# Optimization experiments

Hardware: AMD Instinct MI355X
Metric: run time of the kernel (lower is better)

Reference implementation:

```python
import jax, jax.numpy as jnp
import numpy as np

B, S, D, H, DC, HC = 2, 2048, 1024, 16, 64, 16  # batch, seq, hidden, heads, coord_dim, head_coord_dim
HD = D // H  # head_dim


def setup_inputs() -> dict:
    key = jax.random.key(0)
    ks = jax.random.split(key, 12)
    s = lambda fan_in: 1.0 / np.sqrt(fan_in)
    return {
        "hidden_states": jax.random.normal(ks[0], (B, S, D), jnp.float32),
        "coordinates": jax.random.normal(ks[1], (B, S, DC), jnp.float32),
        # weights stored [in, out] (used as x @ W + b, equivalent to torch Linear)
        "Wv": jax.random.uniform(ks[2], (D, D), jnp.float32, -s(D), s(D)),
        "bv": jax.random.uniform(ks[3], (D,), jnp.float32, -s(D), s(D)),
        "Wc": jax.random.uniform(ks[4], (DC, H * HC), jnp.float32, -s(DC), s(DC)),
        "bc": jax.random.uniform(ks[5], (H * HC,), jnp.float32, -s(DC), s(DC)),
        "Wn": jax.random.uniform(ks[6], (DC, DC), jnp.float32, -s(DC), s(DC)),
        "bn": jax.random.uniform(ks[7], (DC,), jnp.float32, -s(DC), s(DC)),
        "Wo": jax.random.uniform(ks[8], (D, D), jnp.float32, -s(D), s(D)),
        "bo": jax.random.uniform(ks[9], (D,), jnp.float32, -s(D), s(D)),
        "gamma": jax.random.normal(ks[10], (1, H, 1, 1), jnp.float32),
    }


def reference(hidden_states, coordinates, Wv, bv, Wc, bc, Wn, bn, Wo, bo, gamma):
    b, s, _ = hidden_states.shape
    # value: [B,H,S,HD]
    value = (hidden_states @ Wv + bv).reshape(b, s, H, HD).transpose(0, 2, 1, 3)
    # coord heads: [B,H,S,HC]
    z = (coordinates @ Wc + bc).reshape(b, s, H, HC).transpose(0, 2, 1, 3)
    z_sq = jnp.sum(z * z, axis=-1, keepdims=True)  # [B,H,S,1]
    sq_dist = z_sq + jnp.swapaxes(z_sq, -1, -2) - 2.0 * jnp.einsum("bhsc,bhtc->bhst", z, z)
    sq_dist = jnp.maximum(sq_dist, 0.0)
    g = jax.nn.softplus(gamma)  # [1,H,1,1]
    attn = jax.nn.softmax(-g * sq_dist, axis=-1)  # [B,H,S,S]
    out = jnp.einsum("bhst,bhtd->bhsd", attn, value)
    out = out.transpose(0, 2, 1, 3).reshape(b, s, D)
    updated_hidden = out @ Wo + bo
    updated_coords = coordinates @ Wn + bn
    return (updated_hidden, updated_coords)
```

## Files before the change

### kernel.cpp

```cpp
#include <hip/hip_runtime.h>
#include <hip/hip_bf16.h>

typedef short bf16x8 __attribute__((ext_vector_type(8)));
typedef float f32x4 __attribute__((ext_vector_type(4)));
typedef float f32x16 __attribute__((ext_vector_type(16)));
typedef unsigned short u16;
typedef unsigned int u32;

__device__ __forceinline__ u16 f2b(float f) {
  __hip_bfloat16 h = __float2bfloat16(f);
  return *reinterpret_cast<u16*>(&h);
}

#define MFMA16(a, b, c) __builtin_amdgcn_mfma_f32_16x16x32_bf16((a), (b), (c), 0, 0, 0)
#define MFMA32(a, b, c) __builtin_amdgcn_mfma_f32_32x32x16_bf16((a), (b), (c), 0, 0, 0)


__global__ void k_cvt(const float* __restrict__ in, u16* __restrict__ out, int n) {
  int i = (blockIdx.x * 256 + threadIdx.x) * 4;
  if (i >= n) return;
  float4 v = *reinterpret_cast<const float4*>(in + i);
  ushort4 o;
  o.x = f2b(v.x); o.y = f2b(v.y); o.z = f2b(v.z); o.w = f2b(v.w);
  *reinterpret_cast<ushort4*>(out + i) = o;
}

__global__ void k_wT(const float* __restrict__ W, u16* __restrict__ WT) {
  __shared__ float t[64][65];
  int tid = threadIdx.x;
  int r0 = (blockIdx.x & 15) << 6;
  int c0 = (blockIdx.x >> 4) << 6;
#pragma unroll
  for (int rep = 0; rep < 4; ++rep) {
    int e = tid + rep * 256;
    int r = e >> 4, c4 = (e & 15) << 2;
    float4 v = *reinterpret_cast<const float4*>(W + (size_t)(r0 + r) * 1024 + c0 + c4);
    t[r][c4] = v.x; t[r][c4 + 1] = v.y; t[r][c4 + 2] = v.z; t[r][c4 + 3] = v.w;
  }
  __syncthreads();
#pragma unroll
  for (int rep = 0; rep < 4; ++rep) {
    int e = tid + rep * 256;
    int c = e >> 4, r4 = (e & 15) << 2;
    ushort4 o;
    o.x = f2b(t[r4][c]); o.y = f2b(t[r4 + 1][c]);
    o.z = f2b(t[r4 + 2][c]); o.w = f2b(t[r4 + 3][c]);
    *reinterpret_cast<ushort4*>(WT + (size_t)(c0 + c) * 1024 + r0 + r4) = o;
  }
}

__global__ void k_z(const float* __restrict__ C, const float* __restrict__ Wc,
                    const float* __restrict__ bc, u16* __restrict__ Z,
                    float* __restrict__ zsq) {
  int gid = blockIdx.x * 256 + threadIdx.x;
  int bs = gid >> 4, h = gid & 15;
  const float* crow = C + (size_t)bs * 64;
  float acc[16];
#pragma unroll
  for (int c = 0; c < 16; ++c) acc[c] = bc[h * 16 + c];
  for (int k = 0; k < 64; ++k) {
    float cv = crow[k];
    const float* wr = Wc + (size_t)k * 256 + h * 16;
#pragma unroll
    for (int c = 0; c < 16; ++c) acc[c] = fmaf(cv, wr[c], acc[c]);
  }
  float sq = 0.f;
  u16 tmp[16];
#pragma unroll
  for (int c = 0; c < 16; ++c) { sq += acc[c] * acc[c]; tmp[c] = f2b(acc[c]); }
  int b = bs >> 11, s = bs & 2047;
  int bh = (b << 4) + h;
  u16* zr = Z + (((size_t)bh << 11) + s) * 16;
  *reinterpret_cast<uint4*>(zr) = *reinterpret_cast<uint4*>(tmp);
  *reinterpret_cast<uint4*>(zr + 8) = *reinterpret_cast<uint4*>(tmp + 8);
  zsq[((size_t)bh << 11) + s] = sq;
}

template <int OUTM>
__global__ __launch_bounds__(256) void k_gemm(const u16* __restrict__ A,
                                              const u16* __restrict__ BT,
                                              const float* __restrict__ bias,
                                              void* __restrict__ Cout,
                                              int M, int N, int K) {
  __shared__ u16 As[128 * 64];
  __shared__ u16 Bs[64 * 64];
  int nbn = N >> 6;
  int bm = blockIdx.x / nbn, bn = blockIdx.x % nbn;
  int tid = threadIdx.x, lane = tid & 63, w = tid >> 6;
  int wm = w >> 1, wn = w & 1;
  int l15 = lane & 15, lg = lane >> 4;
  int lr = lane >> 3;
  int swc = (lane & 7) ^ lr;

  f32x4 acc[4][2];
#pragma unroll
  for (int mi = 0; mi < 4; ++mi)
#pragma unroll
    for (int ni = 0; ni < 2; ++ni) acc[mi][ni] = (f32x4){0.f, 0.f, 0.f, 0.f};

  const u16* Abase = A + (size_t)(bm * 128) * K + (size_t)(w * 8 + lr) * K + swc * 8;
  const u16* Bbase = BT + (size_t)(bn * 64) * K + (size_t)(w * 8 + lr) * K + swc * 8;
  int rsw = l15 & 7;

  for (int kk0 = 0; kk0 < K; kk0 += 64) {
    __syncthreads();
#pragma unroll
    for (int i = 0; i < 4; ++i)
      __builtin_amdgcn_global_load_lds(
          (const __attribute__((address_space(1))) u32*)(Abase + (size_t)(i * 32) * K + kk0),
          (__attribute__((address_space(3))) u32*)&As[(i * 32 + w * 8) * 64], 16, 0, 0);
#pragma unroll
    for (int i = 0; i < 2; ++i)
      __builtin_amdgcn_global_load_lds(
          (const __attribute__((address_space(1))) u32*)(Bbase + (size_t)(i * 32) * K + kk0),
          (__attribute__((address_space(3))) u32*)&Bs[(i * 32 + w * 8) * 64], 16, 0, 0);
    __syncthreads();
#pragma unroll
    for (int kk = 0; kk < 2; ++kk) {
      bf16x8 af[4], bfr[2];
#pragma unroll
      for (int mi = 0; mi < 4; ++mi) {
        int row = wm * 64 + mi * 16 + l15;
        int ch = (kk * 4 + lg) ^ rsw;
        af[mi] = *reinterpret_cast<const bf16x8*>(&As[row * 64 + ch * 8]);
      }
#pragma unroll
      for (int ni = 0; ni < 2; ++ni) {
        int row = wn * 32 + ni * 16 + l15;
        int ch = (kk * 4 + lg) ^ rsw;
        bfr[ni] = *reinterpret_cast<const bf16x8*>(&Bs[row * 64 + ch * 8]);
      }
#pragma unroll
      for (int mi = 0; mi < 4; ++mi)
#pragma unroll
        for (int ni = 0; ni < 2; ++ni)
          acc[mi][ni] = MFMA16(af[mi], bfr[ni], acc[mi][ni]);
    }
  }
#pragma unroll
  for (int mi = 0; mi < 4; ++mi) {
#pragma unroll
    for (int ni = 0; ni < 2; ++ni) {
      int col = bn * 64 + wn * 32 + ni * 16 + l15;
      float bb = bias[col];
#pragma unroll
      for (int j = 0; j < 4; ++j) {
        int row = bm * 128 + wm * 64 + mi * 16 + lg * 4 + j;
        float v = acc[mi][ni][j] + bb;
        if (OUTM == 0) {
          reinterpret_cast<float*>(Cout)[(size_t)row * N + col] = v;
        } else {
          int b = row >> 11, s = row & 2047, h = col >> 6, hd = col & 63;
          reinterpret_cast<u16*>(Cout)[((((size_t)(b * 16 + h) << 11) | s) << 6) + hd] = f2b(v);
        }
      }
    }
  }
}

__global__ void k_vF(const u16* __restrict__ V, u16* __restrict__ VF) {
  __shared__ u16 t[64][72];
  int tid = threadIdx.x;
  int bh = blockIdx.x >> 5;
  int s0 = (blockIdx.x & 31) << 6;
#pragma unroll
  for (int rep = 0; rep < 2; ++rep) {
    int e = tid + rep * 256;
    int sl = e >> 3, seg = (e & 7) << 3;
    *reinterpret_cast<uint4*>(&t[sl][seg]) =
        *reinterpret_cast<const uint4*>(V + ((size_t)(bh * 2048 + s0 + sl) << 6) + seg);
  }
  __syncthreads();
  int tg0 = (blockIdx.x & 31) << 2;
#pragma unroll
  for (int rep = 0; rep < 2; ++rep) {
    int c = tid + rep * 256;
    int l = c & 63;
    int dh = (c >> 6) & 1;
    int tgl = c >> 7;
    int l31 = l & 31, hi = l >> 5;
    u16 tmp[8];
#pragma unroll
    for (int j = 0; j < 8; ++j) tmp[j] = t[tgl * 16 + hi * 8 + j][dh * 32 + l31];
    size_t off = ((((size_t)bh * 128 + tg0 + tgl) * 2 + dh) << 9) + (l << 3);
    *reinterpret_cast<uint4*>(VF + off) = *reinterpret_cast<uint4*>(tmp);
  }
}

__global__ __launch_bounds__(256, 4) void k_attn(const u16* __restrict__ Z,
                                                 const float* __restrict__ zsq,
                                                 const u16* __restrict__ VF,
                                                 const float* __restrict__ gamma,
                                                 u16* __restrict__ O) {
  __shared__ __align__(16) char smem[18944];
  float* psqf = reinterpret_cast<float*>(smem + 18432);

  int tid = threadIdx.x, lane = tid & 63, w = tid >> 6;
  int l31 = lane & 31, hi = lane >> 5;
  int hi4 = hi << 2, hi8 = hi << 3;
  int th = w >> 1, qh = w & 1, th32 = th << 5;
  int bh = blockIdx.x >> 5, qt = blockIdx.x & 31;
  int q0 = qt << 6;
  int h = bh & 15, bb = bh >> 4;
  float gm = gamma[h];
  float g = (gm > 15.f) ? gm : log1pf(__expf(gm));
  float g2 = g * 1.4426950408889634f;

  const u16* Zb = Z + ((size_t)bh << 11) * 16;
  const float* zsb = zsq + ((size_t)bh << 11);
  const u16* VFb = VF + ((size_t)bh << 17);

  int q = (qh << 5) + l31;
  char* Prow = smem + q * 144;
  u32 psw = ((u32)(q >> 3) & 3u) << 4;

  uint4 zqu = *reinterpret_cast<const uint4*>(Zb + (size_t)(q0 + q) * 16 + hi8);
  zqu.x += 0x00800080u; zqu.y += 0x00800080u;
  zqu.z += 0x00800080u; zqu.w += 0x00800080u;
  bf16x8 zq2 = *reinterpret_cast<bf16x8*>(&zqu);

  bf16x8 aug_b;
  {
    float xq = -zsb[q0 + q];
    u32 xqu = __float_as_uint(xq);
    float xqh = __uint_as_float(xqu & 0xFFFF0000u);
    float xql = xq - xqh;
    u32 w1q = __builtin_amdgcn_perm(__float_as_uint(xql), xqu, 0x07060302u);
    uint4 abu = {0x3F803F80u, w1q, 0u, 0u};
    if (hi) { abu.x = 0u; abu.y = 0u; }
    aug_b = *reinterpret_cast<bf16x8*>(&abu);
  }

  const u16* zap = Zb + (size_t)(th32 + l31) * 16 + hi8;
  const float* xtp = zsb + th32 + l31;
  const u16* vwp = VFb + ((size_t)(th * 2) << 10) + (lane << 3);

  f32x16 oacc0 = {}, oacc1 = {};
  f32x4 psacc = {};

  bf16x8 zA_c = *reinterpret_cast<const bf16x8*>(zap);
  float zs_c = xtp[0];
  bf16x8 vb00_c = *reinterpret_cast<const bf16x8*>(vwp);
  bf16x8 vb10_c = *reinterpret_cast<const bf16x8*>(vwp + 512);

#pragma unroll 2
  for (int tt = 0; tt < 32; ++tt) {
    const int t0 = tt << 6;
    char* Pr = Prow + ((tt & 1) ? 9216 : 0);
    const u16* vtb = vwp + (tt << 12);
    bf16x8 vb01 = *reinterpret_cast<const bf16x8*>(vtb + 1024);
    bf16x8 vb11 = *reinterpret_cast<const bf16x8*>(vtb + 1024 + 512);
    bf16x8 zA_n = zA_c, vb00_n = vb00_c, vb10_n = vb10_c;
    float zs_n = zs_c;
    if (tt < 31) {
      zA_n = *reinterpret_cast<const bf16x8*>(zap + (size_t)(t0 + 64) * 16);
      zs_n = xtp[t0 + 64];
      vb00_n = *reinterpret_cast<const bf16x8*>(vtb + 4096);
      vb10_n = *reinterpret_cast<const bf16x8*>(vtb + 4096 + 512);
    }

    float xt = -zs_c;
    u32 xtu = __float_as_uint(xt);
    float xth = __uint_as_float(xtu & 0xFFFF0000u);
    float xtl = xt - xth;
    u32 w0 = __builtin_amdgcn_perm(__float_as_uint(xtl), xtu, 0x07060302u);
    uint4 aau = {w0, 0x3F803F80u, 0u, 0u};
    if (hi) { aau.x = 0u; aau.y = 0u; }
    bf16x8 aug_a = *reinterpret_cast<bf16x8*>(&aau);

    f32x16 sc = MFMA32(aug_a, aug_b, (f32x16){});
    sc = MFMA32(zA_c, zq2, sc);

#pragma unroll
    for (int g4 = 0; g4 < 4; ++g4) {
      float e0 = fminf(g2 * sc[g4 * 4 + 0], 0.f);
      float e1 = fminf(g2 * sc[g4 * 4 + 1], 0.f);
      float e2 = fminf(g2 * sc[g4 * 4 + 2], 0.f);
      float e3 = fminf(g2 * sc[g4 * 4 + 3], 0.f);
      float p0 = __builtin_amdgcn_exp2f(e0);
      float p1 = __builtin_amdgcn_exp2f(e1);
      float p2 = __builtin_amdgcn_exp2f(e2);
      float p3 = __builtin_amdgcn_exp2f(e3);
      psacc[0] += p0; psacc[1] += p1; psacc[2] += p2; psacc[3] += p3;
      u32 pk0, pk1;
      asm("v_cvt_pk_bf16_f32 %0, %1, %2" : "=v"(pk0) : "v"(p0), "v"(p1));
      asm("v_cvt_pk_bf16_f32 %0, %1, %2" : "=v"(pk1) : "v"(p2), "v"(p3));
      uint2 pkv = {pk0, pk1};
      int tcol = th32 + (g4 << 3) + hi4;
      *reinterpret_cast<uint2*>(Pr + (((u32)(tcol << 1)) ^ psw)) = pkv;
    }

    bf16x8 pa0 = *reinterpret_cast<const bf16x8*>(Pr + (((u32)((th32 + hi8) << 1)) ^ psw));
    bf16x8 pa1 = *reinterpret_cast<const bf16x8*>(Pr + (((u32)((th32 + 16 + hi8) << 1)) ^ psw));

    oacc0 = MFMA32(pa0, vb00_c, oacc0);
    oacc1 = MFMA32(pa0, vb10_c, oacc1);
    oacc0 = MFMA32(pa1, vb01, oacc0);
    oacc1 = MFMA32(pa1, vb11, oacc1);

    zA_c = zA_n; zs_c = zs_n; vb00_c = vb00_n; vb10_c = vb10_n;
  }

  float psum = (psacc[0] + psacc[1]) + (psacc[2] + psacc[3]);

  psum += __shfl_xor(psum, 32, 64);
  __syncthreads();
  if (w >= 2) {
    char* dst = smem + (w - 2) * 8192 + lane * 16;
#pragma unroll
    for (int c = 0; c < 4; ++c) {
      f32x4 v = {oacc0[c * 4 + 0], oacc0[c * 4 + 1], oacc0[c * 4 + 2], oacc0[c * 4 + 3]};
      *reinterpret_cast<f32x4*>(dst + c * 1024) = v;
    }
#pragma unroll
    for (int c = 0; c < 4; ++c) {
      f32x4 v = {oacc1[c * 4 + 0], oacc1[c * 4 + 1], oacc1[c * 4 + 2], oacc1[c * 4 + 3]};
      *reinterpret_cast<f32x4*>(dst + (c + 4) * 1024) = v;
    }
  }
  if (lane < 32) psqf[w * 32 + l31] = psum;
  __syncthreads();
  if (w < 2) {
    const char* src = smem + w * 8192 + lane * 16;
#pragma unroll
    for (int c = 0; c < 4; ++c) {
      f32x4 v = *reinterpret_cast<const f32x4*>(src + c * 1024);
      oacc0[c * 4 + 0] += v[0]; oacc0[c * 4 + 1] += v[1];
      oacc0[c * 4 + 2] += v[2]; oacc0[c * 4 + 3] += v[3];
    }
#pragma unroll
    for (int c = 0; c < 4; ++c) {
      f32x4 v = *reinterpret_cast<const f32x4*>(src + (c + 4) * 1024);
      oacc1[c * 4 + 0] += v[0]; oacc1[c * 4 + 1] += v[1];
      oacc1[c * 4 + 2] += v[2]; oacc1[c * 4 + 3] += v[3];
    }
#pragma unroll
    for (int g4 = 0; g4 < 4; ++g4) {
      f32x4 a = *reinterpret_cast<const f32x4*>(&psqf[qh * 32 + (g4 << 3) + hi4]);
      f32x4 b2 = *reinterpret_cast<const f32x4*>(&psqf[(qh + 2) * 32 + (g4 << 3) + hi4]);
#pragma unroll
      for (int j = 0; j < 4; ++j) {
        float inv = __builtin_amdgcn_rcpf(a[j] + b2[j]);
        int qrow = (g4 << 3) + hi4 + j;
        int srow = q0 + (qh << 5) + qrow;
        u16* orow = O + ((size_t)(bb * 2048 + srow) << 10) + h * 64 + l31;
        orow[0] = f2b(oacc0[g4 * 4 + j] * inv);
        orow[32] = f2b(oacc1[g4 * 4 + j] * inv);
      }
    }
  }
}

__global__ void k_coords(const float* __restrict__ C, const float* __restrict__ Wn,
                         const float* __restrict__ bn, float* __restrict__ out) {
  int gid = blockIdx.x * 256 + threadIdx.x;
  int bs = gid >> 6, c = gid & 63;
  const float* crow = C + (size_t)bs * 64;
  float acc = bn[c];
#pragma unroll 8
  for (int k = 0; k < 64; ++k) acc = fmaf(crow[k], Wn[k * 64 + c], acc);
  out[gid] = acc;
}

extern "C" void kernel_launch(void* const* d_in, const int* in_sizes, int n_in,
                              void* d_out, int out_size, void* d_ws, size_t ws_size,
                              hipStream_t stream) {
  const float* hs     = (const float*)d_in[0];
  const float* coords = (const float*)d_in[1];
  const float* Wv     = (const float*)d_in[2];
  const float* bv     = (const float*)d_in[3];
  const float* Wc     = (const float*)d_in[4];
  const float* bc     = (const float*)d_in[5];
  const float* Wn     = (const float*)d_in[6];
  const float* bn     = (const float*)d_in[7];
  const float* Wo     = (const float*)d_in[8];
  const float* bo     = (const float*)d_in[9];
  const float* gamma  = (const float*)d_in[10];
  float* out_h = (float*)d_out;
  float* out_c = out_h + 4194304;

  char* ws = (char*)d_ws;
  u16*   HSb  = (u16*)(ws + 0);
  u16*   O    = (u16*)(ws + 0);
  u16*   WvT  = (u16*)(ws + 8388608);
  u16*   WoT  = (u16*)(ws + 10485760);
  u16*   Zw   = (u16*)(ws + 12582912);
  float* zsqw = (float*)(ws + 14680064);
  u16*   Vw   = (u16*)(ws + 14942208);
  u16*   VFw  = (u16*)(ws + 23330816);

  k_cvt<<<4096, 256, 0, stream>>>(hs, HSb, 4194304);
  k_wT<<<256, 256, 0, stream>>>(Wv, WvT);
  k_wT<<<256, 256, 0, stream>>>(Wo, WoT);
  k_z<<<256, 256, 0, stream>>>(coords, Wc, bc, Zw, zsqw);
  k_gemm<1><<<512, 256, 0, stream>>>(HSb, WvT, bv, Vw, 4096, 1024, 1024);
  k_vF<<<1024, 256, 0, stream>>>(Vw, VFw);
  k_attn<<<1024, 256, 0, stream>>>(Zw, zsqw, VFw, gamma, O);
  k_gemm<0><<<512, 256, 0, stream>>>(O, WoT, bo, out_h, 4096, 1024, 1024);
  k_coords<<<1024, 256, 0, stream>>>(coords, Wn, bn, out_c);
}
```

Baseline: 121.3 us.

## Fuse prep kernels, fold gamma into Z, and widen GEMM blocks

Merges the hidden-state conversion, both weight transposes, the coordinate-head projection and the coordinate output linear into one launch, cutting launch count from nine to five. The coordinate projection now also writes a gamma-scaled copy of Z and a packed split-bf16 of -g*|z|^2. This lets the attention loop drop its per-element gamma multiply and the per-tile norm splitting, and the query-norm term is computed once by an MFMA. Both GEMMs now run 512 threads per block so each wave holds a smaller accumulator tile. That may raise occupancy but also means fewer MFMAs per LDS load.

```diff
diff --git a/kernel.cpp b/kernel.cpp
--- a/kernel.cpp
+++ b/kernel.cpp
@@ -16,72 +16,107 @@
 #define MFMA32(a, b, c) __builtin_amdgcn_mfma_f32_32x32x16_bf16((a), (b), (c), 0, 0, 0)
 
 
-__global__ void k_cvt(const float* __restrict__ in, u16* __restrict__ out, int n) {
-  int i = (blockIdx.x * 256 + threadIdx.x) * 4;
-  if (i >= n) return;
-  float4 v = *reinterpret_cast<const float4*>(in + i);
-  ushort4 o;
-  o.x = f2b(v.x); o.y = f2b(v.y); o.z = f2b(v.z); o.w = f2b(v.w);
-  *reinterpret_cast<ushort4*>(out + i) = o;
-}
-
-__global__ void k_wT(const float* __restrict__ W, u16* __restrict__ WT) {
+__global__ __launch_bounds__(256) void k_prep(
+    const float* __restrict__ hs, u16* __restrict__ HSb,
+    const float* __restrict__ Wv, u16* __restrict__ WvT,
+    const float* __restrict__ Wo, u16* __restrict__ WoT,
+    const float* __restrict__ C, const float* __restrict__ Wc,
+    const float* __restrict__ bc, const float* __restrict__ gamma,
+    u16* __restrict__ Z, u16* __restrict__ Zg, u32* __restrict__ zghl,
+    const float* __restrict__ Wn, const float* __restrict__ bn,
+    float* __restrict__ outc) {
   __shared__ float t[64][65];
   int tid = threadIdx.x;
-  int r0 = (blockIdx.x & 15) << 6;
-  int c0 = (blockIdx.x >> 4) << 6;
-#pragma unroll
-  for (int rep = 0; rep < 4; ++rep) {
-    int e = tid + rep * 256;
-    int r = e >> 4, c4 = (e & 15) << 2;
-    float4 v = *reinterpret_cast<const float4*>(W + (size_t)(r0 + r) * 1024 + c0 + c4);
-    t[r][c4] = v.x; t[r][c4 + 1] = v.y; t[r][c4 + 2] = v.z; t[r][c4 + 3] = v.w;
-  }
-  __syncthreads();
-#pragma unroll
-  for (int rep = 0; rep < 4; ++rep) {
-    int e = tid + rep * 256;
-    int c = e >> 4, r4 = (e & 15) << 2;
+  int blk = blockIdx.x;
+
+  if (blk < 4096) {
+    int i = (blk * 256 + tid) * 4;
+    float4 v = *reinterpret_cast<const float4*>(hs + i);
     ushort4 o;
-    o.x = f2b(t[r4][c]); o.y = f2b(t[r4 + 1][c]);
-    o.z = f2b(t[r4 + 2][c]); o.w = f2b(t[r4 + 3][c]);
-    *reinterpret_cast<ushort4*>(WT + (size_t)(c0 + c) * 1024 + r0 + r4) = o;
-  }
-}
-
-__global__ void k_z(const float* __restrict__ C, const float* __restrict__ Wc,
-                    const float* __restrict__ bc, u16* __restrict__ Z,
-                    float* __restrict__ zsq) {
-  int gid = blockIdx.x * 256 + threadIdx.x;
-  int bs = gid >> 4, h = gid & 15;
-  const float* crow = C + (size_t)bs * 64;
-  float acc[16];
-#pragma unroll
-  for (int c = 0; c < 16; ++c) acc[c] = bc[h * 16 + c];
-  for (int k = 0; k < 64; ++k) {
-    float cv = crow[k];
-    const float* wr = Wc + (size_t)k * 256 + h * 16;
-#pragma unroll
-    for (int c = 0; c < 16; ++c) acc[c] = fmaf(cv, wr[c], acc[c]);
-  }
-  float sq = 0.f;
-  u16 tmp[16];
-#pragma unroll
-  for (int c = 0; c < 16; ++c) { sq += acc[c] * acc[c]; tmp[c] = f2b(acc[c]); }
-  int b = bs >> 11, s = bs & 2047;
-  int bh = (b << 4) + h;
-  u16* zr = Z + (((size_t)bh << 11) + s) * 16;
-  *reinterpret_cast<uint4*>(zr) = *reinterpret_cast<uint4*>(tmp);
-  *reinterpret_cast<uint4*>(zr + 8) = *reinterpret_cast<uint4*>(tmp + 8);
-  zsq[((size_t)bh << 11) + s] = sq;
+    o.x = f2b(v.x); o.y = f2b(v.y); o.z = f2b(v.z); o.w = f2b(v.w);
+    *reinterpret_cast<ushort4*>(HSb + i) = o;
+    return;
+  }
+  if (blk < 4608) {
+    const float* W = (blk < 4352) ? Wv : Wo;
+    u16* WT = (blk < 4352) ? WvT : WoT;
+    int bid = (blk < 4352) ? blk - 4096 : blk - 4352;
+    int r0 = (bid & 15) << 6, c0 = (bid >> 4) << 6;
+#pragma unroll
+    for (int rep = 0; rep < 4; ++rep) {
+      int e = tid + rep * 256;
+      int r = e >> 4, c4 = (e & 15) << 2;
+      float4 v = *reinterpret_cast<const float4*>(W + (size_t)(r0 + r) * 1024 + c0 + c4);
+      t[r][c4] = v.x; t[r][c4 + 1] = v.y; t[r][c4 + 2] = v.z; t[r][c4 + 3] = v.w;
+    }
+    __syncthreads();
+#pragma unroll
+    for (int rep = 0; rep < 4; ++rep) {
+      int e = tid + rep * 256;
+      int c = e >> 4, r4 = (e & 15) << 2;
+      ushort4 o;
+      o.x = f2b(t[r4][c]); o.y = f2b(t[r4 + 1][c]);
+      o.z = f2b(t[r4 + 2][c]); o.w = f2b(t[r4 + 3][c]);
+      *reinterpret_cast<ushort4*>(WT + (size_t)(c0 + c) * 1024 + r0 + r4) = o;
+    }
+    return;
+  }
+  if (blk < 4864) {
+    int gid = (blk - 4608) * 256 + tid;
+    int bs = gid >> 4, h = gid & 15;
+    float gm = gamma[h];
+    float g = (gm > 15.f) ? gm : log1pf(__expf(gm));
+    float g2 = g * 1.4426950408889634f;
+    float tg2 = 2.f * g2;
+    const float* crow = C + (size_t)bs * 64;
+    float acc[16];
+#pragma unroll
+    for (int c = 0; c < 16; ++c) acc[c] = bc[h * 16 + c];
+    for (int k = 0; k < 64; ++k) {
+      float cv = crow[k];
+      const float* wr = Wc + (size_t)k * 256 + h * 16;
+#pragma unroll
+      for (int c = 0; c < 16; ++c) acc[c] = fmaf(cv, wr[c], acc[c]);
+    }
+    float sq = 0.f;
+    u16 tz[16], tg[16];
+#pragma unroll
+    for (int c = 0; c < 16; ++c) {
+      sq += acc[c] * acc[c];
+      tz[c] = f2b(acc[c]);
+      tg[c] = f2b(tg2 * acc[c]);
+    }
+    float x = -g2 * sq;
+    u32 xu = __float_as_uint(x);
+    float xh = __uint_as_float(xu & 0xFFFF0000u);
+    u32 packed = (xu >> 16) | ((u32)f2b(x - xh) << 16);
+    int b = bs >> 11, s = bs & 2047;
+    int bh = (b << 4) + h;
+    size_t ro = (((size_t)bh << 11) + s) * 16;
+    *reinterpret_cast<uint4*>(Z + ro) = *reinterpret_cast<uint4*>(tz);
+    *reinterpret_cast<uint4*>(Z + ro + 8) = *reinterpret_cast<uint4*>(tz + 8);
+    *reinterpret_cast<uint4*>(Zg + ro) = *reinterpret_cast<uint4*>(tg);
+    *reinterpret_cast<uint4*>(Zg + ro + 8) = *reinterpret_cast<uint4*>(tg + 8);
+    zghl[((size_t)bh << 11) + s] = packed;
+    return;
+  }
+  {
+    int gid = (blk - 4864) * 256 + tid;
+    int bs = gid >> 6, c = gid & 63;
+    const float* crow = C + (size_t)bs * 64;
+    float acc = bn[c];
+#pragma unroll 8
+    for (int k = 0; k < 64; ++k) acc = fmaf(crow[k], Wn[k * 64 + c], acc);
+    outc[gid] = acc;
+  }
 }
 
 template <int OUTM>
-__global__ __launch_bounds__(256) void k_gemm(const u16* __restrict__ A,
-                                              const u16* __restrict__ BT,
-                                              const float* __restrict__ bias,
-                                              void* __restrict__ Cout,
-                                              int M, int N, int K) {
+__global__ __launch_bounds__(512, 4) void k_gemm(const u16* __restrict__ A,
+                                                 const u16* __restrict__ BT,
+                                                 const float* __restrict__ bias,
+                                                 void* __restrict__ Cout,
+                                                 int M, int N, int K) {
   __shared__ u16 As[128 * 64];
   __shared__ u16 Bs[64 * 64];
   int nbn = N >> 6;
@@ -92,60 +127,53 @@
   int lr = lane >> 3;
   int swc = (lane & 7) ^ lr;
 
-  f32x4 acc[4][2];
-#pragma unroll
-  for (int mi = 0; mi < 4; ++mi)
+  f32x4 acc[2][2];
+#pragma unroll
+  for (int mi = 0; mi < 2; ++mi)
 #pragma unroll
     for (int ni = 0; ni < 2; ++ni) acc[mi][ni] = (f32x4){0.f, 0.f, 0.f, 0.f};
 
-  const u16* Abase = A + (size_t)(bm * 128) * K + (size_t)(w * 8 + lr) * K + swc * 8;
-  const u16* Bbase = BT + (size_t)(bn * 64) * K + (size_t)(w * 8 + lr) * K + swc * 8;
+  const u16* Abase = A + (size_t)(bm * 128 + w * 8 + lr) * K + swc * 8;
+  const u16* Bbase = BT + (size_t)(bn * 64 + w * 8 + lr) * K + swc * 8;
   int rsw = l15 & 7;
 
   for (int kk0 = 0; kk0 < K; kk0 += 64) {
     __syncthreads();
 #pragma unroll
-    for (int i = 0; i < 4; ++i)
-      __builtin_amdgcn_global_load_lds(
-          (const __attribute__((address_space(1))) u32*)(Abase + (size_t)(i * 32) * K + kk0),
-          (__attribute__((address_space(3))) u32*)&As[(i * 32 + w * 8) * 64], 16, 0, 0);
-#pragma unroll
     for (int i = 0; i < 2; ++i)
       __builtin_amdgcn_global_load_lds(
-          (const __attribute__((address_space(1))) u32*)(Bbase + (size_t)(i * 32) * K + kk0),
-          (__attribute__((address_space(3))) u32*)&Bs[(i * 32 + w * 8) * 64], 16, 0, 0);
+          (const __attribute__((address_space(1))) u32*)(Abase + (size_t)(i * 64) * K + kk0),
+          (__attribute__((address_space(3))) u32*)&As[(i * 64 + w * 8) * 64], 16, 0, 0);
+    __builtin_amdgcn_global_load_lds(
+        (const __attribute__((address_space(1))) u32*)(Bbase + kk0),
+        (__attribute__((address_space(3))) u32*)&Bs[(w * 8) * 64], 16, 0, 0);
     __syncthreads();
 #pragma unroll
     for (int kk = 0; kk < 2; ++kk) {
-      bf16x8 af[4], bfr[2];
-#pragma unroll
-      for (int mi = 0; mi < 4; ++mi) {
-        int row = wm * 64 + mi * 16 + l15;
-        int ch = (kk * 4 + lg) ^ rsw;
-        af[mi] = *reinterpret_cast<const bf16x8*>(&As[row * 64 + ch * 8]);
-      }
-#pragma unroll
-      for (int ni = 0; ni < 2; ++ni) {
-        int row = wn * 32 + ni * 16 + l15;
-        int ch = (kk * 4 + lg) ^ rsw;
-        bfr[ni] = *reinterpret_cast<const bf16x8*>(&Bs[row * 64 + ch * 8]);
-      }
-#pragma unroll
-      for (int mi = 0; mi < 4; ++mi)
+      int ch = (kk * 4 + lg) ^ rsw;
+      bf16x8 af[2], bfr[2];
+#pragma unroll
+      for (int mi = 0; mi < 2; ++mi)
+        af[mi] = *reinterpret_cast<const bf16x8*>(&As[(wm * 32 + mi * 16 + l15) * 64 + ch * 8]);
+#pragma unroll
+      for (int ni = 0; ni < 2; ++ni)
+        bfr[ni] = *reinterpret_cast<const bf16x8*>(&Bs[(wn * 32 + ni * 16 + l15) * 64 + ch * 8]);
+#pragma unroll
+      for (int mi = 0; mi < 2; ++mi)
 #pragma unroll
         for (int ni = 0; ni < 2; ++ni)
           acc[mi][ni] = MFMA16(af[mi], bfr[ni], acc[mi][ni]);
     }
   }
 #pragma unroll
-  for (int mi = 0; mi < 4; ++mi) {
+  for (int mi = 0; mi < 2; ++mi) {
 #pragma unroll
     for (int ni = 0; ni < 2; ++ni) {
       int col = bn * 64 + wn * 32 + ni * 16 + l15;
       float bb = bias[col];
 #pragma unroll
       for (int j = 0; j < 4; ++j) {
-        int row = bm * 128 + wm * 64 + mi * 16 + lg * 4 + j;
+        int row = bm * 128 + wm * 32 + mi * 16 + lg * 4 + j;
         float v = acc[mi][ni][j] + bb;
         if (OUTM == 0) {
           reinterpret_cast<float*>(Cout)[(size_t)row * N + col] = v;
@@ -188,9 +216,9 @@
 }
 
 __global__ __launch_bounds__(256, 4) void k_attn(const u16* __restrict__ Z,
-                                                 const float* __restrict__ zsq,
+                                                 const u16* __restrict__ Zg,
+                                                 const u32* __restrict__ zghl,
                                                  const u16* __restrict__ VF,
-                                                 const float* __restrict__ gamma,
                                                  u16* __restrict__ O) {
   __shared__ __align__(16) char smem[18944];
   float* psqf = reinterpret_cast<float*>(smem + 18432);
@@ -202,44 +230,37 @@
   int bh = blockIdx.x >> 5, qt = blockIdx.x & 31;
   int q0 = qt << 6;
   int h = bh & 15, bb = bh >> 4;
-  float gm = gamma[h];
-  float g = (gm > 15.f) ? gm : log1pf(__expf(gm));
-  float g2 = g * 1.4426950408889634f;
 
   const u16* Zb = Z + ((size_t)bh << 11) * 16;
-  const float* zsb = zsq + ((size_t)bh << 11);
+  const u16* Zgb = Zg + ((size_t)bh << 11) * 16;
+  const u32* ghl = zghl + ((size_t)bh << 11);
   const u16* VFb = VF + ((size_t)bh << 17);
 
   int q = (qh << 5) + l31;
   char* Prow = smem + q * 144;
   u32 psw = ((u32)(q >> 3) & 3u) << 4;
 
-  uint4 zqu = *reinterpret_cast<const uint4*>(Zb + (size_t)(q0 + q) * 16 + hi8);
-  zqu.x += 0x00800080u; zqu.y += 0x00800080u;
-  zqu.z += 0x00800080u; zqu.w += 0x00800080u;
-  bf16x8 zq2 = *reinterpret_cast<bf16x8*>(&zqu);
-
-  bf16x8 aug_b;
-  {
-    float xq = -zsb[q0 + q];
-    u32 xqu = __float_as_uint(xq);
-    float xqh = __uint_as_float(xqu & 0xFFFF0000u);
-    float xql = xq - xqh;
-    u32 w1q = __builtin_amdgcn_perm(__float_as_uint(xql), xqu, 0x07060302u);
-    uint4 abu = {0x3F803F80u, w1q, 0u, 0u};
-    if (hi) { abu.x = 0u; abu.y = 0u; }
-    aug_b = *reinterpret_cast<bf16x8*>(&abu);
-  }
+  bf16x8 zq2 = *reinterpret_cast<const bf16x8*>(Zgb + (size_t)(q0 + q) * 16 + hi8);
+
+  u32 gq = ghl[q0 + q];
+  uint4 abu = {0x3F803F80u, gq, 0u, 0u};
+  if (hi) { abu.x = 0u; abu.y = 0u; }
+  bf16x8 aug_b = *reinterpret_cast<bf16x8*>(&abu);
+
+  uint4 aqu = {0u, 0x3F803F80u, 0u, 0u};
+  if (hi) aqu.y = 0u;
+  bf16x8 aug_q = *reinterpret_cast<bf16x8*>(&aqu);
+  f32x16 qpart = MFMA32(aug_q, aug_b, (f32x16){});
 
   const u16* zap = Zb + (size_t)(th32 + l31) * 16 + hi8;
-  const float* xtp = zsb + th32 + l31;
+  const u32* xtp = ghl + th32 + l31;
   const u16* vwp = VFb + ((size_t)(th * 2) << 10) + (lane << 3);
 
   f32x16 oacc0 = {}, oacc1 = {};
   f32x4 psacc = {};
 
   bf16x8 zA_c = *reinterpret_cast<const bf16x8*>(zap);
-  float zs_c = xtp[0];
+  u32 zhl_c = xtp[0];
   bf16x8 vb00_c = *reinterpret_cast<const bf16x8*>(vwp);
   bf16x8 vb10_c = *reinterpret_cast<const bf16x8*>(vwp + 512);
 
@@ -251,32 +272,26 @@
     bf16x8 vb01 = *reinterpret_cast<const bf16x8*>(vtb + 1024);
     bf16x8 vb11 = *reinterpret_cast<const bf16x8*>(vtb + 1024 + 512);
     bf16x8 zA_n = zA_c, vb00_n = vb00_c, vb10_n = vb10_c;
-    float zs_n = zs_c;
+    u32 zhl_n = zhl_c;
     if (tt < 31) {
       zA_n = *reinterpret_cast<const bf16x8*>(zap + (size_t)(t0 + 64) * 16);
-      zs_n = xtp[t0 + 64];
+      zhl_n = xtp[t0 + 64];
       vb00_n = *reinterpret_cast<const bf16x8*>(vtb + 4096);
       vb10_n = *reinterpret_cast<const bf16x8*>(vtb + 4096 + 512);
     }
 
-    float xt = -zs_c;
-    u32 xtu = __float_as_uint(xt);
-    float xth = __uint_as_float(xtu & 0xFFFF0000u);
-    float xtl = xt - xth;
-    u32 w0 = __builtin_amdgcn_perm(__float_as_uint(xtl), xtu, 0x07060302u);
-    uint4 aau = {w0, 0x3F803F80u, 0u, 0u};
-    if (hi) { aau.x = 0u; aau.y = 0u; }
+    uint4 aau = {hi ? 0u : zhl_c, 0u, 0u, 0u};
     bf16x8 aug_a = *reinterpret_cast<bf16x8*>(&aau);
 
-    f32x16 sc = MFMA32(aug_a, aug_b, (f32x16){});
+    f32x16 sc = MFMA32(aug_a, aug_b, qpart);
     sc = MFMA32(zA_c, zq2, sc);
 
 #pragma unroll
     for (int g4 = 0; g4 < 4; ++g4) {
-      float e0 = fminf(g2 * sc[g4 * 4 + 0], 0.f);
-      float e1 = fminf(g2 * sc[g4 * 4 + 1], 0.f);
-      float e2 = fminf(g2 * sc[g4 * 4 + 2], 0.f);
-      float e3 = fminf(g2 * sc[g4 * 4 + 3], 0.f);
+      float e0 = fminf(sc[g4 * 4 + 0], 0.f);
+      float e1 = fminf(sc[g4 * 4 + 1], 0.f);
+      float e2 = fminf(sc[g4 * 4 + 2], 0.f);
+      float e3 = fminf(sc[g4 * 4 + 3], 0.f);
       float p0 = __builtin_amdgcn_exp2f(e0);
       float p1 = __builtin_amdgcn_exp2f(e1);
       float p2 = __builtin_amdgcn_exp2f(e2);
@@ -298,7 +313,7 @@
     oacc0 = MFMA32(pa1, vb01, oacc0);
     oacc1 = MFMA32(pa1, vb11, oacc1);
 
-    zA_c = zA_n; zs_c = zs_n; vb00_c = vb00_n; vb10_c = vb10_n;
+    zA_c = zA_n; zhl_c = zhl_n; vb00_c = vb00_n; vb10_c = vb10_n;
   }
 
   float psum = (psacc[0] + psacc[1]) + (psacc[2] + psacc[3]);
@@ -349,17 +364,6 @@
       }
     }
   }
-}
-
-__global__ void k_coords(const float* __restrict__ C, const float* __restrict__ Wn,
-                         const float* __restrict__ bn, float* __restrict__ out) {
-  int gid = blockIdx.x * 256 + threadIdx.x;
-  int bs = gid >> 6, c = gid & 63;
-  const float* crow = C + (size_t)bs * 64;
-  float acc = bn[c];
-#pragma unroll 8
-  for (int k = 0; k < 64; ++k) acc = fmaf(crow[k], Wn[k * 64 + c], acc);
-  out[gid] = acc;
 }
 
 extern "C" void kernel_launch(void* const* d_in, const int* in_sizes, int n_in,
@@ -385,17 +389,15 @@
   u16*   WvT  = (u16*)(ws + 8388608);
   u16*   WoT  = (u16*)(ws + 10485760);
   u16*   Zw   = (u16*)(ws + 12582912);
-  float* zsqw = (float*)(ws + 14680064);
-  u16*   Vw   = (u16*)(ws + 14942208);
-  u16*   VFw  = (u16*)(ws + 23330816);
-
-  k_cvt<<<4096, 256, 0, stream>>>(hs, HSb, 4194304);
-  k_wT<<<256, 256, 0, stream>>>(Wv, WvT);
-  k_wT<<<256, 256, 0, stream>>>(Wo, WoT);
-  k_z<<<256, 256, 0, stream>>>(coords, Wc, bc, Zw, zsqw);
-  k_gemm<1><<<512, 256, 0, stream>>>(HSb, WvT, bv, Vw, 4096, 1024, 1024);
+  u16*   Zgw  = (u16*)(ws + 14680064);
+  u32*   zghl = (u32*)(ws + 16777216);
+  u16*   Vw   = (u16*)(ws + 17039360);
+  u16*   VFw  = (u16*)(ws + 25427968);
+
+  k_prep<<<5888, 256, 0, stream>>>(hs, HSb, Wv, WvT, Wo, WoT, coords, Wc, bc,
+                                   gamma, Zw, Zgw, zghl, Wn, bn, out_c);
+  k_gemm<1><<<512, 512, 0, stream>>>(HSb, WvT, bv, Vw, 4096, 1024, 1024);
   k_vF<<<1024, 256, 0, stream>>>(Vw, VFw);
-  k_attn<<<1024, 256, 0, stream>>>(Zw, zsqw, VFw, gamma, O);
-  k_gemm<0><<<512, 256, 0, stream>>>(O, WoT, bo, out_h, 4096, 1024, 1024);
-  k_coords<<<1024, 256, 0, stream>>>(coords, Wn, bn, out_c);
-}
+  k_attn<<<1024, 256, 0, stream>>>(Zw, Zgw, zghl, VFw, O);
+  k_gemm<0><<<512, 512, 0, stream>>>(O, WoT, bo, out_h, 4096, 1024, 1024);
+}
```

After: 187.9 us. +54.9%, slower.
